# Performance work log

Measured on AMD Instinct MI355X. Metric: run time of the kernel, lower is better.

## Reference

```python
import jax, jax.numpy as jnp
import numpy as np
import math

N, H, D_MODEL = 2048, 16, 2048
D_K = D_MODEL // H
D_FF = 4 * D_MODEL
EPS = 1e-5


def _layernorm(x, alpha, beta):
    # torch: mean/var over dim=1 (=feature dim for 2D input), unbiased=False
    m = jnp.mean(x, axis=1, keepdims=True)
    v = jnp.var(x, axis=1, keepdims=True)
    return (x - m) / jnp.sqrt(v + EPS) * alpha + beta


def setup_inputs() -> dict:
    key = jax.random.key(0)
    ks = jax.random.split(key, 12)
    s = 0.02  # weight init scale
    return {
        "X": jax.random.normal(ks[0], (N, D_MODEL), jnp.float32),
        "Wq": jax.random.normal(ks[1], (H, D_MODEL, D_K), jnp.float32) * s,
        "bq": jax.random.normal(ks[2], (H, D_K), jnp.float32) * s,
        "Wk": jax.random.normal(ks[3], (H, D_MODEL, D_K), jnp.float32) * s,
        "bk": jax.random.normal(ks[4], (H, D_K), jnp.float32) * s,
        "Wv": jax.random.normal(ks[5], (H, D_MODEL, D_K), jnp.float32) * s,
        "bv": jax.random.normal(ks[6], (H, D_K), jnp.float32) * s,
        "alpha1": jnp.ones((N, D_MODEL), jnp.float32),
        "beta1": jnp.zeros((N, D_MODEL), jnp.float32),
        "W1": jax.random.normal(ks[7], (D_MODEL, D_FF), jnp.float32) * s,
        "b1": jax.random.normal(ks[8], (D_FF,), jnp.float32) * s,
        "W2": jax.random.normal(ks[9], (D_FF, D_MODEL), jnp.float32) * s,
        "b2": jax.random.normal(ks[10], (D_MODEL,), jnp.float32) * s,
        "alpha2": jnp.ones((N, D_MODEL), jnp.float32),
        "beta2": jnp.zeros((N, D_MODEL), jnp.float32),
    }


def reference(X, Wq, bq, Wk, bk, Wv, bv, alpha1, beta1, W1, b1, W2, b2, alpha2, beta2):
    # --- Multi-headed self-attention (h per-head linears fused as stacked weights) ---
    Q = jnp.einsum('nd,hdk->hnk', X, Wq) + bq[:, None, :]  # (H, N, D_K)
    K = jnp.einsum('nd,hdk->hnk', X, Wk) + bk[:, None, :]
    V = jnp.einsum('nd,hdk->hnk', X, Wv) + bv[:, None, :]
    scores = jnp.einsum('hnk,hmk->hnm', Q, K) / math.sqrt(D_K)  # (H, N, N)
    A = jax.nn.softmax(scores, axis=-1)  # softmax over keys (torch dim=1 of 2D)
    O = jnp.einsum('hnm,hmk->hnk', A, V)  # (H, N, D_K)
    attn = jnp.transpose(O, (1, 0, 2)).reshape(N, D_MODEL)  # concat heads on dim=1
    # --- Add & Norm 1 (dropout is identity at inference) ---
    h1 = _layernorm(X + attn, alpha1, beta1)
    # --- FFN ---
    ffn = jnp.maximum(h1 @ W1 + b1, 0.0) @ W2 + b2
    # --- Add & Norm 2 ---
    return _layernorm(h1 + ffn, alpha2, beta2)
```

## Files before the change

kernel.cpp:

```cpp
#include <hip/hip_runtime.h>
#include <hip/hip_bf16.h>

#define N_TOK 2048
#define DMODEL 2048
#define NH 16
#define DK 128
#define DFF 8192

typedef __attribute__((ext_vector_type(8))) short short8;
typedef __attribute__((ext_vector_type(4))) short s16x4;
typedef __attribute__((ext_vector_type(4))) float f32x4;

__device__ __forceinline__ short f2bf(float f) {
    unsigned int x = __builtin_bit_cast(unsigned int, f);
    unsigned int r = (x + 0x7fffu + ((x >> 16) & 1u)) >> 16;
    return (short)r;
}
__device__ __forceinline__ float bf2f(short s) {
    unsigned int u = ((unsigned int)(unsigned short)s) << 16;
    return __builtin_bit_cast(float, u);
}

__global__ __launch_bounds__(256) void cast_f32_bf16(const float* __restrict__ in,
                                                     short* __restrict__ out, int n8) {
    int i = blockIdx.x * 256 + threadIdx.x;
    if (i >= n8) return;
    const float4* p = (const float4*)in + (size_t)i * 2;
    float4 a = p[0], b = p[1];
    short8 o;
    o[0] = f2bf(a.x); o[1] = f2bf(a.y); o[2] = f2bf(a.z); o[3] = f2bf(a.w);
    o[4] = f2bf(b.x); o[5] = f2bf(b.y); o[6] = f2bf(b.z); o[7] = f2bf(b.w);
    *(short8*)(out + (size_t)i * 8) = o;
}

template <typename TIN>
__global__ __launch_bounds__(256) void transpose_cast(const TIN* __restrict__ in,
                                                      short* __restrict__ out,
                                                      int R, int C, long sIn, long sOut) {
    __shared__ float t[64][65];
    in  += (long)blockIdx.z * sIn;
    out += (long)blockIdx.z * sOut;
    const int tid = threadIdx.x;
    long r0 = (long)blockIdx.y * 64, c0 = (long)blockIdx.x * 64;
    if constexpr (sizeof(TIN) == 4) {
#pragma unroll
        for (int i = 0; i < 4; i++) {
            int r = (tid >> 4) + i * 16;
            int c = (tid & 15) * 4;
            float4 v = *(const float4*)((const float*)in + (r0 + r) * (long)C + c0 + c);
            t[r][c + 0] = v.x; t[r][c + 1] = v.y; t[r][c + 2] = v.z; t[r][c + 3] = v.w;
        }
    } else {
#pragma unroll
        for (int i = 0; i < 2; i++) {
            int r = (tid >> 3) + i * 32;
            int c = (tid & 7) * 8;
            short8 v = *(const short8*)((const short*)in + (r0 + r) * (long)C + c0 + c);
#pragma unroll
            for (int j = 0; j < 8; j++) t[r][c + j] = bf2f(v[j]);
        }
    }
    __syncthreads();
#pragma unroll
    for (int p = 0; p < 2; p++) {
        int c = (tid >> 3) + p * 32;
        int r8 = (tid & 7) * 8;
        short8 v;
#pragma unroll
        for (int j = 0; j < 8; j++) v[j] = f2bf(t[r8 + j][c]);
        *(short8*)(out + (c0 + c) * (long)R + r0 + r8) = v;
    }
}

__device__ __forceinline__ void gld_lds16(const void* g, void* l) {
    __builtin_amdgcn_global_load_lds(
        (const __attribute__((address_space(1))) void*)g,
        (__attribute__((address_space(3))) void*)l, 16, 0, 0);
}

#define VM8 asm volatile("s_waitcnt vmcnt(8)" ::: "memory")
#define VM0 asm volatile("s_waitcnt vmcnt(0)" ::: "memory")
#define VMNONE ((void)0)

#define PHASE(BUF, MH, NHI, RA, RBNH, STAGE_STMT, VMSTMT)                       \
  {                                                                             \
    if (RA) {                                                                   \
      _Pragma("unroll") for (int mp = 0; mp < 4; mp++)                          \
        _Pragma("unroll") for (int kk = 0; kk < 2; kk++) {                      \
          int rowA = wr * 128 + (MH) * 64 + mp * 16 + fr;                       \
          af[mp][kk] = *(const short8*)((const char*)lds + (BUF) * 65536 +      \
                         rowA * 128 + (((kk * 4 + fq) ^ (rowA & 7)) << 4));     \
        }                                                                       \
    }                                                                           \
    if ((RBNH) < 2) {                                                           \
      _Pragma("unroll") for (int np = 0; np < 2; np++)                          \
        _Pragma("unroll") for (int kk = 0; kk < 2; kk++) {                      \
          int rowB = wc * 64 + (RBNH) * 32 + np * 16 + fr;                      \
          bf[(RBNH) & 1][np][kk] =                                              \
              *(const short8*)((const char*)lds + (BUF) * 65536 + 32768 +       \
                  rowB * 128 + (((kk * 4 + fq) ^ (rowB & 7)) << 4));            \
        }                                                                       \
    }                                                                           \
    STAGE_STMT;                                                                 \
    __builtin_amdgcn_s_barrier();                                               \
    __builtin_amdgcn_s_setprio(1);                                              \
    _Pragma("unroll") for (int mp = 0; mp < 4; mp++)                            \
      _Pragma("unroll") for (int np = 0; np < 2; np++)                          \
        _Pragma("unroll") for (int kk = 0; kk < 2; kk++)                        \
          acc[(MH) * 4 + mp][(NHI) * 2 + np] =                                  \
              __builtin_amdgcn_mfma_f32_16x16x32_bf16(                          \
                  af[mp][kk], bf[NHI][np][kk], acc[(MH) * 4 + mp][(NHI) * 2 + np],\
                  0, 0, 0);                                                     \
    __builtin_amdgcn_s_setprio(0);                                              \
    VMSTMT;                                                                     \
    __builtin_amdgcn_s_barrier();                                               \
  }

template <int MODE>
__global__ __launch_bounds__(512, 2) void gemm256(const short* __restrict__ A,
                                                  const short* __restrict__ Bt,
                                                  void* __restrict__ Cv,
                                                  const float* __restrict__ b0,
                                                  const float* __restrict__ b1,
                                                  const float* __restrict__ b2,
                                                  int Ktot, int TM) {
    __shared__ short lds[65536];
    const int tid = threadIdx.x, lane = tid & 63, w = tid >> 6;
    const int T = gridDim.x, bid = blockIdx.x;
    const int vbid = (bid & 7) * (T >> 3) + (bid >> 3);
    const int mt = vbid % TM;
    const int rest = vbid / TM;
    int nt = rest, z = 0;
    if (MODE == 2) { nt = rest & 7; z = rest >> 3; }
    const long brow = (long)mt * 256, bcol = (long)nt * 256;
    const short* Ab = A + (MODE == 2 ? (long)z * 2048 : 0);
    const short* Bb = Bt + (MODE == 2 ? (long)z * 2048 : 0);

    auto stageA = [&](int kt, int buf, int mh) {
#pragma unroll
        for (int j = 0; j < 2; j++) {
            int row = mh * 64 + j * 128 + (tid >> 3);
            int g = (lane & 7) ^ (row & 7);
            gld_lds16((const char*)(Ab + (brow + row) * (long)Ktot + (long)kt * 64) + g * 16,
                      (char*)lds + buf * 65536 + mh * 8192 + j * 16384 + w * 1024 + lane * 16);
        }
    };
    auto stageB = [&](int kt, int buf, int nh) {
#pragma unroll
        for (int j = 0; j < 2; j++) {
            int s = 2 * j + (w >> 2);
            int rin = (w & 3) * 8 + (lane >> 3);
            int row = s * 64 + nh * 32 + rin;
            int g = (lane & 7) ^ (row & 7);
            gld_lds16((const char*)(Bb + (bcol + row) * (long)Ktot + (long)kt * 64) + g * 16,
                      (char*)lds + buf * 65536 + 32768 + j * 16384 + (w >> 2) * 8192 +
                          nh * 4096 + (w & 3) * 1024 + lane * 16);
        }
    };

    const int wr = w >> 2, wc = w & 3;
    const int fr = lane & 15, fq = lane >> 4;
    f32x4 acc[8][4] = {};
    short8 af[4][2], bf[2][2][2];

    stageA(0, 0, 0); stageB(0, 0, 0); stageB(0, 0, 1); stageA(0, 0, 1);
    stageA(1, 1, 0); stageB(1, 1, 0); stageB(1, 1, 1); stageA(1, 1, 1);
    VM8;
    __builtin_amdgcn_s_barrier();

    for (int i = 0; i < 15; i++) {
        const int kn = 2 * i + 2;
        PHASE(0, 0, 0, 1, 0, {}, VMNONE)
        PHASE(0, 0, 1, 0, 1, { stageA(kn, 0, 0); stageB(kn, 0, 0); }, VMNONE)
        PHASE(0, 1, 0, 1, 2, { stageB(kn, 0, 1); }, VMNONE)
        PHASE(0, 1, 1, 0, 2, { stageA(kn, 0, 1); }, VM8)
        PHASE(1, 0, 0, 1, 0, {}, VMNONE)
        PHASE(1, 0, 1, 0, 1, { stageA(kn + 1, 1, 0); stageB(kn + 1, 1, 0); }, VMNONE)
        PHASE(1, 1, 0, 1, 2, { stageB(kn + 1, 1, 1); }, VMNONE)
        PHASE(1, 1, 1, 0, 2, { stageA(kn + 1, 1, 1); }, VM8)
    }
    PHASE(0, 0, 0, 1, 0, {}, VMNONE)
    PHASE(0, 0, 1, 0, 1, {}, VMNONE)
    PHASE(0, 1, 0, 1, 2, {}, VMNONE)
    PHASE(0, 1, 1, 0, 2, {}, VM0)
    PHASE(1, 0, 0, 1, 0, {}, VMNONE)
    PHASE(1, 0, 1, 0, 1, {}, VMNONE)
    PHASE(1, 1, 0, 1, 2, {}, VMNONE)
    PHASE(1, 1, 1, 0, 2, {}, VMNONE)

    const long crow0 = brow + wr * 128, ccol0 = bcol + wc * 64;
#pragma unroll
    for (int n = 0; n < 4; n++) {
        const long col = ccol0 + (n >> 1) * 32 + (n & 1) * 16 + fr;
        float bval = 0.f;
        if (MODE == 0) {
            const float* bp = (col >> 11) == 0 ? b0 : (col >> 11) == 1 ? b1 : b2;
            bval = bp[col & 2047];
        } else if (MODE == 1) bval = b0[col];
#pragma unroll
        for (int m = 0; m < 8; m++) {
#pragma unroll
            for (int r = 0; r < 4; r++) {
                const long row = crow0 + (m >> 2) * 64 + (m & 3) * 16 + fq * 4 + r;
                float v = acc[m][n][r] + bval;
                if (MODE == 0) {
                    const long slab = col >> 7;
                    ((short*)Cv)[slab * (2048L * 128) + row * 128 + (col & 127)] = f2bf(v);
                } else if (MODE == 1) {
                    ((short*)Cv)[row * 8192 + col] = f2bf(fmaxf(v, 0.f));
                } else {
                    ((short*)Cv)[(long)z * (2048L * 2048) + row * 2048 + col] = f2bf(v);
                }
            }
        }
    }
}

__global__ __launch_bounds__(512, 2) void attn_flash(const short* __restrict__ Q,
                                                     const short* __restrict__ Kc,
                                                     const short* __restrict__ VT,
                                                     short* __restrict__ O) {
    __shared__ short lds[73728];
    const int tid = threadIdx.x, lane = tid & 63, w = tid >> 6;
    const int bid = blockIdx.x;
    const int vid = (bid & 7) * 32 + (bid >> 3);
    const int h = vid >> 4, qt = vid & 15;
    const int fr = lane & 15, fq = lane >> 4;
    const long qbase = (long)qt * 128 + w * 16;
    const short* Qh = Q  + (long)h * N_TOK * DK;
    const short* Kh = Kc + (long)h * N_TOK * DK;
    const short* Vh = VT + (long)h * DK * N_TOK;
    short* Pw = lds + 65536 + w * 1024;

    short8 qf[4];
#pragma unroll
    for (int c = 0; c < 4; c++)
        qf[c] = *(const short8*)(Qh + (qbase + fr) * DK + c * 32 + fq * 8);

    float mrow = -1e30f, lrow = 0.f;
    f32x4 oacc[8] = {};
    const float C1 = 0.08838834764831845f * 1.4426950408889634f;
    const float THR = 16.f;

    int wr_off[4], rd_off[2];
#pragma unroll
    for (int jc = 0; jc < 4; jc++)
        wr_off[jc] = (fr * 64 + jc * 16 + fq * 4) ^ ((fr & 7) << 3);
#pragma unroll
    for (int kc = 0; kc < 2; kc++)
        rd_off[kc] = (fr * 64 + kc * 32 + fq * 8) ^ ((fr & 7) << 3);
    int colKb[4], colVb[2];
#pragma unroll
    for (int c = 0; c < 4; c++) colKb[c] = (c * 64 + fq * 16) ^ ((fr & 7) << 4);
#pragma unroll
    for (int kc = 0; kc < 2; kc++) colVb[kc] = (kc * 64 + fq * 16) ^ ((fr & 7) << 4);

    auto stageK = [&](int kvt) {
        const int buf = kvt & 3;
        const char* Kg = (const char*)(Kh + (long)kvt * 64 * DK);
        char* Kd = (char*)lds + buf * 16384;
#pragma unroll
        for (int i = 0; i < 2; i++) {
            int a = (w * 2 + i) * 1024 + (lane << 4);
            int src = a ^ (((a >> 8) & 7) << 4);
            gld_lds16(Kg + src, Kd + (w * 2 + i) * 1024);
        }
    };
    auto stageV = [&](int kvt) {
        const int buf = kvt & 3;
        char* Vd = (char*)lds + 65536 + buf * 16384;
#pragma unroll
        for (int i = 0; i < 2; i++) {
            int a = (w * 2 + i) * 1024 + (lane << 4);
            int row = a >> 7;
            int inner = (a & 127) ^ ((row & 7) << 4);
            const char* src = (const char*)Vh + ((long)row * N_TOK + (long)kvt * 64) * 2 + inner;
            gld_lds16(src, Vd + (w * 2 + i) * 1024);
        }
    };

    const int NT = N_TOK / 64;
    stageK(0); stageV(0); stageK(1); stageV(1); stageK(2); stageV(2); stageK(3);
    asm volatile("s_waitcnt vmcnt(12)" ::: "memory");
    __builtin_amdgcn_s_barrier();
    __builtin_amdgcn_sched_barrier(0);

    for (int t = 0; t < NT; t++) {
        const char* Kcb = (const char*)lds + (t & 3) * 16384;
        f32x4 s[4] = {};
#pragma unroll
        for (int jc = 0; jc < 4; jc++) {
            const char* rb = Kcb + (jc * 16 + fr) * 256;
#pragma unroll
            for (int c = 0; c < 4; c++) {
                short8 kf = *(const short8*)(rb + colKb[c]);
                s[jc] = __builtin_amdgcn_mfma_f32_16x16x32_bf16(kf, qf[c], s[jc], 0, 0, 0);
            }
        }

        float tm = -1e30f;
#pragma unroll
        for (int jc = 0; jc < 4; jc++)
#pragma unroll
            for (int r = 0; r < 4; r++) tm = fmaxf(tm, s[jc][r]);
        tm = fmaxf(tm, __shfl_xor(tm, 16));
        tm = fmaxf(tm, __shfl_xor(tm, 32));
        if (!__all(tm <= mrow + THR)) {
            float nm = fmaxf(mrow, tm);
            float resc = exp2f(C1 * (mrow - nm));
            mrow = nm;
            lrow *= resc;
#pragma unroll
            for (int f = 0; f < 8; f++)
#pragma unroll
                for (int r = 0; r < 4; r++) oacc[f][r] *= resc;
        }
        float sum = 0.f;
#pragma unroll
        for (int jc = 0; jc < 4; jc++)
#pragma unroll
            for (int r = 0; r < 4; r++) {
                float p = exp2f(C1 * (s[jc][r] - mrow));
                s[jc][r] = p;
                sum += p;
            }
        sum += __shfl_xor(sum, 16);
        sum += __shfl_xor(sum, 32);
        lrow += sum;

#pragma unroll
        for (int jc = 0; jc < 4; jc++) {
            s16x4 pk;
            pk[0] = f2bf(s[jc][0]); pk[1] = f2bf(s[jc][1]);
            pk[2] = f2bf(s[jc][2]); pk[3] = f2bf(s[jc][3]);
            *(s16x4*)(Pw + wr_off[jc]) = pk;
        }
        short8 pa[2];
#pragma unroll
        for (int kc = 0; kc < 2; kc++)
            pa[kc] = *(const short8*)(Pw + rd_off[kc]);

        if (t < NT - 4) asm volatile("s_waitcnt vmcnt(8)" ::: "memory");
        else            asm volatile("s_waitcnt vmcnt(0)" ::: "memory");
        __builtin_amdgcn_sched_barrier(0);
        __builtin_amdgcn_s_barrier();
        __builtin_amdgcn_sched_barrier(0);

        const char* Vcb = (const char*)lds + 65536 + (t & 3) * 16384;
#pragma unroll
        for (int f = 0; f < 8; f++) {
            const char* rb = Vcb + (f * 16 + fr) * 128;
#pragma unroll
            for (int kc = 0; kc < 2; kc++) {
                short8 vf = *(const short8*)(rb + colVb[kc]);
                oacc[f] = __builtin_amdgcn_mfma_f32_16x16x32_bf16(vf, pa[kc], oacc[f], 0, 0, 0);
            }
        }

        if (t + 4 < NT) stageK(t + 4);
        if (t + 3 < NT) stageV(t + 3);
    }

    const float inv = 1.f / lrow;
    const long row = qbase + fr;
#pragma unroll
    for (int f = 0; f < 8; f++) {
        s16x4 ob;
        ob[0] = f2bf(oacc[f][0] * inv); ob[1] = f2bf(oacc[f][1] * inv);
        ob[2] = f2bf(oacc[f][2] * inv); ob[3] = f2bf(oacc[f][3] * inv);
        *(s16x4*)(O + row * (long)DMODEL + h * DK + f * 16 + fq * 4) = ob;
    }
}

__global__ __launch_bounds__(256) void add_ln1(const float* __restrict__ A,
                                               const short* __restrict__ B,
                                               const float* __restrict__ alpha,
                                               const float* __restrict__ beta,
                                               float* __restrict__ out,
                                               short* __restrict__ outbf) {
    const int row = blockIdx.x, t = threadIdx.x;
    const long base = (long)row * DMODEL;
    float x[8];
    float s = 0.f, q = 0.f;
#pragma unroll
    for (int i = 0; i < 2; i++) {
        long off = base + (long)(t + i * 256) * 4;
        float4 va = *(const float4*)(A + off);
        s16x4 vb = *(const s16x4*)(B + off);
        float xa[4] = { va.x, va.y, va.z, va.w };
#pragma unroll
        for (int j = 0; j < 4; j++) {
            float v = xa[j] + bf2f(vb[j]);
            x[i * 4 + j] = v;
            s += v; q += v * v;
        }
    }
#pragma unroll
    for (int o = 1; o < 64; o <<= 1) { s += __shfl_xor(s, o); q += __shfl_xor(q, o); }
    __shared__ float red[8];
    if ((t & 63) == 0) { red[t >> 6] = s; red[4 + (t >> 6)] = q; }
    __syncthreads();
    s = red[0] + red[1] + red[2] + red[3];
    q = red[4] + red[5] + red[6] + red[7];
    const float mean = s * (1.f / DMODEL);
    const float var = q * (1.f / DMODEL) - mean * mean;
    const float rstd = rsqrtf(var + 1e-5f);
#pragma unroll
    for (int i = 0; i < 2; i++) {
        long off = base + (long)(t + i * 256) * 4;
        float4 al = *(const float4*)(alpha + off);
        float4 be = *(const float4*)(beta + off);
        float a[4] = { al.x, al.y, al.z, al.w };
        float b[4] = { be.x, be.y, be.z, be.w };
#pragma unroll
        for (int j = 0; j < 4; j++) {
            float o2 = (x[i * 4 + j] - mean) * rstd * a[j] + b[j];
            out[off + j] = o2;
            outbf[off + j] = f2bf(o2);
        }
    }
}

__global__ __launch_bounds__(256) void add_ln2_red(const float* __restrict__ H1,
                                                   const short* __restrict__ F4,
                                                   const float* __restrict__ b2,
                                                   const float* __restrict__ alpha,
                                                   const float* __restrict__ beta,
                                                   float* __restrict__ out) {
    const int row = blockIdx.x, t = threadIdx.x;
    const long base = (long)row * DMODEL;
    const long SL = (long)N_TOK * DMODEL;
    float x[8];
    float s = 0.f, q = 0.f;
#pragma unroll
    for (int i = 0; i < 2; i++) {
        long off = base + (long)(t + i * 256) * 4;
        int col = (t + i * 256) * 4;
        float4 a  = *(const float4*)(H1 + off);
        s16x4 f0 = *(const s16x4*)(F4 + off);
        s16x4 f1 = *(const s16x4*)(F4 + off + SL);
        s16x4 f2 = *(const s16x4*)(F4 + off + 2 * SL);
        s16x4 f3 = *(const s16x4*)(F4 + off + 3 * SL);
        float4 bb = *(const float4*)(b2 + col);
        float xa[4] = { a.x + bb.x, a.y + bb.y, a.z + bb.z, a.w + bb.w };
#pragma unroll
        for (int j = 0; j < 4; j++) {
            float v = xa[j] + bf2f(f0[j]) + bf2f(f1[j]) + bf2f(f2[j]) + bf2f(f3[j]);
            x[i * 4 + j] = v;
            s += v; q += v * v;
        }
    }
#pragma unroll
    for (int o = 1; o < 64; o <<= 1) { s += __shfl_xor(s, o); q += __shfl_xor(q, o); }
    __shared__ float red[8];
    if ((t & 63) == 0) { red[t >> 6] = s; red[4 + (t >> 6)] = q; }
    __syncthreads();
    s = red[0] + red[1] + red[2] + red[3];
    q = red[4] + red[5] + red[6] + red[7];
    const float mean = s * (1.f / DMODEL);
    const float var = q * (1.f / DMODEL) - mean * mean;
    const float rstd = rsqrtf(var + 1e-5f);
#pragma unroll
    for (int i = 0; i < 2; i++) {
        long off = base + (long)(t + i * 256) * 4;
        float4 al = *(const float4*)(alpha + off);
        float4 be = *(const float4*)(beta + off);
        float a[4] = { al.x, al.y, al.z, al.w };
        float b[4] = { be.x, be.y, be.z, be.w };
#pragma unroll
        for (int j = 0; j < 4; j++)
            out[off + j] = (x[i * 4 + j] - mean) * rstd * a[j] + b[j];
    }
}

extern "C" void kernel_launch(void* const* d_in, const int* in_sizes, int n_in,
                              void* d_out, int out_size, void* d_ws, size_t ws_size,
                              hipStream_t stream) {
    const float* X      = (const float*)d_in[0];
    const float* Wq     = (const float*)d_in[1];
    const float* bq     = (const float*)d_in[2];
    const float* Wk     = (const float*)d_in[3];
    const float* bk     = (const float*)d_in[4];
    const float* Wv     = (const float*)d_in[5];
    const float* bv     = (const float*)d_in[6];
    const float* alpha1 = (const float*)d_in[7];
    const float* beta1  = (const float*)d_in[8];
    const float* W1     = (const float*)d_in[9];
    const float* b1     = (const float*)d_in[10];
    const float* W2     = (const float*)d_in[11];
    const float* b2     = (const float*)d_in[12];
    const float* alpha2 = (const float*)d_in[13];
    const float* beta2  = (const float*)d_in[14];
    float* out = (float*)d_out;

    char* ws = (char*)d_ws;
    size_t off = 0;
    auto alloc = [&](size_t bytes) -> void* {
        void* p = ws + off;
        off += (bytes + 255) & ~(size_t)255;
        return p;
    };
    short* XBF   = (short*)alloc(2048UL * 2048 * 2);
    short* WQKVT = (short*)alloc(48UL * 128 * 2048 * 2);
    short* W1T   = (short*)alloc(8192UL * 2048 * 2);
    short* W2T   = (short*)alloc(2048UL * 8192 * 2);
    short* QKV   = (short*)alloc(48UL * 2048 * 128 * 2);
    short* VT    = (short*)alloc(16UL * 128 * 2048 * 2);
    short* ATTN  = (short*)alloc(2048UL * 2048 * 2);
    float* H1    = (float*)alloc(2048UL * 2048 * 4);
    short* H1BF  = (short*)alloc(2048UL * 2048 * 2);
    short* G     = (short*)alloc(2048UL * 8192 * 2);
    short* F4 = XBF;

    cast_f32_bf16<<<2048, 256, 0, stream>>>(X, XBF, 2048 * 2048 / 8);
    transpose_cast<float><<<dim3(2, 32, 16), 256, 0, stream>>>(Wq, WQKVT,                    2048, 128, 2048L * 128, 128L * 2048);
    transpose_cast<float><<<dim3(2, 32, 16), 256, 0, stream>>>(Wk, WQKVT + 16L * 128 * 2048, 2048, 128, 2048L * 128, 128L * 2048);
    transpose_cast<float><<<dim3(2, 32, 16), 256, 0, stream>>>(Wv, WQKVT + 32L * 128 * 2048, 2048, 128, 2048L * 128, 128L * 2048);
    transpose_cast<float><<<dim3(128, 32, 1), 256, 0, stream>>>(W1, W1T, 2048, 8192, 0, 0);
    transpose_cast<float><<<dim3(32, 128, 1), 256, 0, stream>>>(W2, W2T, 8192, 2048, 0, 0);

    gemm256<0><<<192, 512, 0, stream>>>(XBF, WQKVT, QKV, bq, bk, bv, 2048, 8);

    transpose_cast<__hip_bfloat16><<<dim3(2, 32, 16), 256, 0, stream>>>(
        (const __hip_bfloat16*)(QKV + 32L * 2048 * 128), VT, 2048, 128, 2048L * 128, 128L * 2048);

    attn_flash<<<256, 512, 0, stream>>>(QKV, QKV + 16L * 2048 * 128, VT, ATTN);

    add_ln1<<<2048, 256, 0, stream>>>(X, ATTN, alpha1, beta1, H1, H1BF);

    gemm256<1><<<256, 512, 0, stream>>>(H1BF, W1T, G, b1, nullptr, nullptr, 2048, 8);
    gemm256<2><<<256, 512, 0, stream>>>(G, W2T, F4, nullptr, nullptr, nullptr, 8192, 8);

    add_ln2_red<<<2048, 256, 0, stream>>>(H1, F4, b2, alpha2, beta2, out);
}
```

Before: 364.4 us.

## Shrink attention LDS to double buffering and keep residual H1 only in bf16

The flash-attention kernel's K/V staging drops from four LDS buffers to two, cutting shared memory from about 144KB to 80KB, and launch bounds now ask for 4 waves per SIMD. Waits are re-placed for the shallower prefetch. Separately, add_ln1 no longer writes an fp32 H1 copy, and add_ln2 reads the bf16 H1 residual, which removes 16MB of fp32 write and read traffic. The risks are less latency hiding from the shallower prefetch and bf16 rounding of the residual path.

```diff
diff --git a/kernel.cpp b/kernel.cpp
--- a/kernel.cpp
+++ b/kernel.cpp
@@ -216,11 +216,11 @@
     }
 }
 
-__global__ __launch_bounds__(512, 2) void attn_flash(const short* __restrict__ Q,
+__global__ __launch_bounds__(512, 4) void attn_flash(const short* __restrict__ Q,
                                                      const short* __restrict__ Kc,
                                                      const short* __restrict__ VT,
                                                      short* __restrict__ O) {
-    __shared__ short lds[73728];
+    __shared__ short lds[40960];
     const int tid = threadIdx.x, lane = tid & 63, w = tid >> 6;
     const int bid = blockIdx.x;
     const int vid = (bid & 7) * 32 + (bid >> 3);
@@ -230,7 +230,7 @@
     const short* Qh = Q  + (long)h * N_TOK * DK;
     const short* Kh = Kc + (long)h * N_TOK * DK;
     const short* Vh = VT + (long)h * DK * N_TOK;
-    short* Pw = lds + 65536 + w * 1024;
+    short* Pw = lds + 32768 + w * 1024;
 
     short8 qf[4];
 #pragma unroll
@@ -256,7 +256,7 @@
     for (int kc = 0; kc < 2; kc++) colVb[kc] = (kc * 64 + fq * 16) ^ ((fr & 7) << 4);
 
     auto stageK = [&](int kvt) {
-        const int buf = kvt & 3;
+        const int buf = kvt & 1;
         const char* Kg = (const char*)(Kh + (long)kvt * 64 * DK);
         char* Kd = (char*)lds + buf * 16384;
 #pragma unroll
@@ -267,8 +267,8 @@
         }
     };
     auto stageV = [&](int kvt) {
-        const int buf = kvt & 3;
-        char* Vd = (char*)lds + 65536 + buf * 16384;
+        const int buf = kvt & 1;
+        char* Vd = (char*)lds + 32768 + buf * 16384;
 #pragma unroll
         for (int i = 0; i < 2; i++) {
             int a = (w * 2 + i) * 1024 + (lane << 4);
@@ -280,13 +280,18 @@
     };
 
     const int NT = N_TOK / 64;
-    stageK(0); stageV(0); stageK(1); stageV(1); stageK(2); stageV(2); stageK(3);
-    asm volatile("s_waitcnt vmcnt(12)" ::: "memory");
+    stageK(0); stageV(0); stageK(1);
+    asm volatile("s_waitcnt vmcnt(4)" ::: "memory");
     __builtin_amdgcn_s_barrier();
     __builtin_amdgcn_sched_barrier(0);
 
     for (int t = 0; t < NT; t++) {
-        const char* Kcb = (const char*)lds + (t & 3) * 16384;
+        if (t > 0) {
+            if (t == NT - 1) asm volatile("s_waitcnt vmcnt(2)" ::: "memory");
+            else             asm volatile("s_waitcnt vmcnt(4)" ::: "memory");
+            __builtin_amdgcn_sched_barrier(0);
+        }
+        const char* Kcb = (const char*)lds + (t & 1) * 16384;
         f32x4 s[4] = {};
 #pragma unroll
         for (int jc = 0; jc < 4; jc++) {
@@ -340,13 +345,13 @@
         for (int kc = 0; kc < 2; kc++)
             pa[kc] = *(const short8*)(Pw + rd_off[kc]);
 
-        if (t < NT - 4) asm volatile("s_waitcnt vmcnt(8)" ::: "memory");
-        else            asm volatile("s_waitcnt vmcnt(0)" ::: "memory");
+        if (t == NT - 1) asm volatile("s_waitcnt vmcnt(0)" ::: "memory");
+        else             asm volatile("s_waitcnt vmcnt(2)" ::: "memory");
         __builtin_amdgcn_sched_barrier(0);
         __builtin_amdgcn_s_barrier();
         __builtin_amdgcn_sched_barrier(0);
 
-        const char* Vcb = (const char*)lds + 65536 + (t & 3) * 16384;
+        const char* Vcb = (const char*)lds + 32768 + (t & 1) * 16384;
 #pragma unroll
         for (int f = 0; f < 8; f++) {
             const char* rb = Vcb + (f * 16 + fr) * 128;
@@ -357,8 +362,8 @@
             }
         }
 
-        if (t + 4 < NT) stageK(t + 4);
-        if (t + 3 < NT) stageV(t + 3);
+        if (t + 1 < NT) stageV(t + 1);
+        if (t + 2 < NT) stageK(t + 2);
     }
 
     const float inv = 1.f / lrow;
@@ -376,7 +381,6 @@
                                                const short* __restrict__ B,
                                                const float* __restrict__ alpha,
                                                const float* __restrict__ beta,
-                                               float* __restrict__ out,
                                                short* __restrict__ outbf) {
     const int row = blockIdx.x, t = threadIdx.x;
     const long base = (long)row * DMODEL;
@@ -412,16 +416,15 @@
         float4 be = *(const float4*)(beta + off);
         float a[4] = { al.x, al.y, al.z, al.w };
         float b[4] = { be.x, be.y, be.z, be.w };
-#pragma unroll
-        for (int j = 0; j < 4; j++) {
-            float o2 = (x[i * 4 + j] - mean) * rstd * a[j] + b[j];
-            out[off + j] = o2;
-            outbf[off + j] = f2bf(o2);
-        }
-    }
-}
-
-__global__ __launch_bounds__(256) void add_ln2_red(const float* __restrict__ H1,
+        s16x4 ob;
+#pragma unroll
+        for (int j = 0; j < 4; j++)
+            ob[j] = f2bf((x[i * 4 + j] - mean) * rstd * a[j] + b[j]);
+        *(s16x4*)(outbf + off) = ob;
+    }
+}
+
+__global__ __launch_bounds__(256) void add_ln2_red(const short* __restrict__ H1,
                                                    const short* __restrict__ F4,
                                                    const float* __restrict__ b2,
                                                    const float* __restrict__ alpha,
@@ -436,16 +439,16 @@
     for (int i = 0; i < 2; i++) {
         long off = base + (long)(t + i * 256) * 4;
         int col = (t + i * 256) * 4;
-        float4 a  = *(const float4*)(H1 + off);
+        s16x4 a  = *(const s16x4*)(H1 + off);
         s16x4 f0 = *(const s16x4*)(F4 + off);
         s16x4 f1 = *(const s16x4*)(F4 + off + SL);
         s16x4 f2 = *(const s16x4*)(F4 + off + 2 * SL);
         s16x4 f3 = *(const s16x4*)(F4 + off + 3 * SL);
         float4 bb = *(const float4*)(b2 + col);
-        float xa[4] = { a.x + bb.x, a.y + bb.y, a.z + bb.z, a.w + bb.w };
+        float ba[4] = { bb.x, bb.y, bb.z, bb.w };
 #pragma unroll
         for (int j = 0; j < 4; j++) {
-            float v = xa[j] + bf2f(f0[j]) + bf2f(f1[j]) + bf2f(f2[j]) + bf2f(f3[j]);
+            float v = bf2f(a[j]) + ba[j] + bf2f(f0[j]) + bf2f(f1[j]) + bf2f(f2[j]) + bf2f(f3[j]);
             x[i * 4 + j] = v;
             s += v; q += v * v;
         }
@@ -507,7 +510,6 @@
     short* QKV   = (short*)alloc(48UL * 2048 * 128 * 2);
     short* VT    = (short*)alloc(16UL * 128 * 2048 * 2);
     short* ATTN  = (short*)alloc(2048UL * 2048 * 2);
-    float* H1    = (float*)alloc(2048UL * 2048 * 4);
     short* H1BF  = (short*)alloc(2048UL * 2048 * 2);
     short* G     = (short*)alloc(2048UL * 8192 * 2);
     short* F4 = XBF;
@@ -526,10 +528,10 @@
 
     attn_flash<<<256, 512, 0, stream>>>(QKV, QKV + 16L * 2048 * 128, VT, ATTN);
 
-    add_ln1<<<2048, 256, 0, stream>>>(X, ATTN, alpha1, beta1, H1, H1BF);
+    add_ln1<<<2048, 256, 0, stream>>>(X, ATTN, alpha1, beta1, H1BF);
 
     gemm256<1><<<256, 512, 0, stream>>>(H1BF, W1T, G, b1, nullptr, nullptr, 2048, 8);
     gemm256<2><<<256, 512, 0, stream>>>(G, W2T, F4, nullptr, nullptr, nullptr, 8192, 8);
 
-    add_ln2_red<<<2048, 256, 0, stream>>>(H1, F4, b2, alpha2, beta2, out);
-}
+    add_ln2_red<<<2048, 256, 0, stream>>>(H1BF, F4, b2, alpha2, beta2, out);
+}
```

Result: faster. 354.2 us (-2.8%).
